# Kernel optimization log

Measured on AMD Instinct MI355X. Metric: run time of the kernel, lower is better.

## Reference

```python
import jax, jax.numpy as jnp
import numpy as np

NEG_MASK = -999.0  # matches masked_fill_(-999) in the torch source

def setup_inputs() -> dict:
    key = jax.random.key(0)
    ks = jax.random.split(key, 8)
    B, N, D = 4, 2048, 768      # batch, nodes, in_dim
    H, Do = 6, 128              # att_head, out_dim (D == H*Do)
    feat_in = jax.random.normal(ks[0], (B, N, D), dtype=jnp.float32)
    adj = jax.random.randint(ks[1], (B, N, N), 0, 2).astype(jnp.int32)
    W = jax.random.normal(ks[2], (H, D, Do), dtype=jnp.float32) * (1.0 / np.sqrt(D))
    b = jnp.zeros((Do,), dtype=jnp.float32)
    w_src = jax.random.normal(ks[3], (H, Do, 1), dtype=jnp.float32) * (1.0 / np.sqrt(Do))
    w_dst = jax.random.normal(ks[4], (H, Do, 1), dtype=jnp.float32) * (1.0 / np.sqrt(Do))
    H_w = jax.random.normal(ks[5], (D, D), dtype=jnp.float32) * (1.0 / np.sqrt(D))
    H_b = jnp.zeros((D,), dtype=jnp.float32)
    return {"feat_in": feat_in, "adj": adj, "W": W, "b": b,
            "w_src": w_src, "w_dst": w_dst, "H_w": H_w, "H_b": H_b}

def reference(feat_in, adj, W, b, w_src, w_dst, H_w, H_b):
    leaky_alpha = 0.2
    B, N, D = feat_in.shape
    Hh = W.shape[0]
    # per-head projection: [B, H, N, Do]
    h = jnp.einsum('bni,hio->bhno', feat_in, W)
    th = jnp.tanh(h)
    attn_src = jnp.einsum('bhno,hoz->bhnz', th, w_src)  # [B,H,N,1]
    attn_dst = jnp.einsum('bhno,hoz->bhnz', th, w_dst)  # [B,H,N,1]
    # additive scores: src_i + dst_j -> [B,H,N,N]
    attn = attn_src + jnp.swapaxes(attn_dst, -1, -2)
    attn = jnp.where(attn >= 0, attn, leaky_alpha * attn)
    mask = (adj == 0)[:, None, :, :]  # [B,1,N,N]
    attn = jnp.where(mask, NEG_MASK, attn)
    attn = jax.nn.softmax(attn, axis=-1)
    feat_out = jnp.einsum('bhnm,bhmo->bhno', attn, h) + b  # [B,H,N,Do]
    feat_out = jnp.swapaxes(feat_out, 1, 2).reshape(B, N, -1)  # [B,N,H*Do]
    feat_out = jax.nn.elu(feat_out)
    gate = jax.nn.sigmoid(feat_in @ H_w.T + H_b)
    out = gate * feat_out + (1.0 - gate) * feat_in
    return out
```

## Files before the change

kernel.cpp:

```cpp
#include <hip/hip_runtime.h>
#include <hip/hip_bf16.h>

#define B_ 4
#define N_ 2048
#define D_ 768
#define H_ 6
#define Do_ 128
#define M_ (B_*N_)
#define C2_ (2*D_)
#define SROW 49152

typedef __attribute__((ext_vector_type(8))) short bf16x8;
typedef __attribute__((ext_vector_type(4))) float f32x4;
typedef __attribute__((ext_vector_type(4))) int int4v;
typedef __attribute__((ext_vector_type(2))) int int2v;
typedef __attribute__((ext_vector_type(4))) float float4v;
typedef __attribute__((ext_vector_type(4))) unsigned short ushort4v;

__device__ __forceinline__ float b2f(short s){
    unsigned u = ((unsigned)(unsigned short)s) << 16;
    return __builtin_bit_cast(float, u);
}
__device__ __forceinline__ short f2b(float f){
    unsigned u = __builtin_bit_cast(unsigned, f);
    unsigned r = (u + 0x7fffu + ((u >> 16) & 1u)) >> 16;
    return (short)r;
}
__device__ __forceinline__ int pk2(float a, float b){
    unsigned ua = __builtin_bit_cast(unsigned, a) + 0x8000u;
    unsigned ub = __builtin_bit_cast(unsigned, b) + 0x8000u;
    return (int)__builtin_amdgcn_perm(ub, ua, 0x07060302u);
}
__device__ __forceinline__ float fast_tanh(float x){
    float a = fabsf(x);
    float e = __expf(-2.0f * a);
    float t = (1.0f - e) / (1.0f + e);
    return copysignf(t, x);
}

#define HT_IDX(bh, n, o) ((((size_t)((bh)*64 + ((n) >> 5))*128 + (o))*32) + ((n) & 31))

__global__ __launch_bounds__(256) void k_prep_pack(const float* __restrict__ W,
                                                   const float* __restrict__ Hw,
                                                   const int* __restrict__ adj,
                                                   short* __restrict__ bmat,
                                                   unsigned char* __restrict__ pk){
    int bid = blockIdx.x, t = threadIdx.x;
    if (bid < C2_){
        int c = bid;
        if (c < D_){
            int hd = c >> 7, o = c & 127;
            const float* wp = W + hd*D_*Do_ + o;
            for (int k = t; k < D_; k += 256) bmat[c*D_ + k] = f2b(wp[k*Do_]);
        } else {
            int d = c - D_;
            const float* hp = Hw + d*D_;
            for (int k = t; k < D_; k += 256) bmat[c*D_ + k] = f2b(hp[k]);
        }
    } else {
        int g = (bid - C2_)*256 + t;
        const int* ap = adj + (size_t)g*8;
        int4v a0 = *(const int4v*)ap;
        int4v a1 = *(const int4v*)(ap + 4);
        unsigned by = 0;
        #pragma unroll
        for (int i = 0; i < 4; i++){
            by |= (a0[i] ? 1u : 0u) << i;
            by |= (a1[i] ? 1u : 0u) << (i + 4);
        }
        pk[g] = (unsigned char)by;
    }
}

__global__ __launch_bounds__(256) void k_gemm(const float* __restrict__ A,
                                              const short* __restrict__ Bm,
                                              short* __restrict__ ht,
                                              float* outg){
    __shared__ short As[128][72];
    __shared__ short Bs[128][72];
    int lid = blockIdx.x;
    int xcd = lid & 7, s = lid >> 3;
    int bx = s >> 3, by = xcd*8 + (s & 7);
    int tid = threadIdx.x;
    int mBase = by * 128, cBase = bx * 128;
    int wave = tid >> 6, lane = tid & 63, q = lane >> 4, nL = lane & 15;
    int wr = (wave >> 1) * 64, wc = (wave & 1) * 64;
    f32x4 acc[4][4] = {};
    for (int kk = 0; kk < D_; kk += 64){
        __syncthreads();
        #pragma unroll
        for (int i = 0; i < 8; i++){
            int idx = tid + i*256;
            int row = idx >> 4, c4 = (idx & 15) * 4;
            float4v av = *(const float4v*)&A[(mBase+row)*D_ + kk + c4];
            int2v w; w[0] = pk2(av[0], av[1]); w[1] = pk2(av[2], av[3]);
            *(int2v*)&As[row][c4] = w;
        }
        #pragma unroll
        for (int i = 0; i < 4; i++){
            int idx = tid + i*256;
            int row = idx >> 3, cs = (idx & 7) * 8;
            *(int4v*)&Bs[row][cs] = *(const int4v*)&Bm[(cBase+row)*D_ + kk + cs];
        }
        __syncthreads();
        #pragma unroll
        for (int k2 = 0; k2 < 64; k2 += 32){
            bf16x8 aF[4], bF[4];
            #pragma unroll
            for (int rt = 0; rt < 4; rt++) aF[rt] = *(const bf16x8*)&As[wr + rt*16 + nL][k2 + q*8];
            #pragma unroll
            for (int ct = 0; ct < 4; ct++) bF[ct] = *(const bf16x8*)&Bs[wc + ct*16 + nL][k2 + q*8];
            #pragma unroll
            for (int rt = 0; rt < 4; rt++)
                #pragma unroll
                for (int ct = 0; ct < 4; ct++)
                    acc[rt][ct] = __builtin_amdgcn_mfma_f32_16x16x32_bf16(aF[rt], bF[ct], acc[rt][ct], 0, 0, 0);
        }
    }
    if (cBase < D_){
        int hd = cBase >> 7;
        #pragma unroll
        for (int rt = 0; rt < 4; rt++){
            #pragma unroll
            for (int ct = 0; ct < 4; ct++){
                int o  = (wc + ct*16 + nL) & 127;
                int m0 = mBase + wr + rt*16 + q*4;
                int b = m0 >> 11, n0 = m0 & 2047;
                int bh = b*H_ + hd;
                ushort4v v;
                #pragma unroll
                for (int r = 0; r < 4; r++) v[r] = (unsigned short)f2b(acc[rt][ct][r]);
                *(ushort4v*)&ht[HT_IDX(bh, n0, o)] = v;
            }
        }
    } else {
        __syncthreads();
        int dQ = cBase - D_ + wc;
        float* Ts = (float*)As + wave*1088;
        int row = lane >> 2, cbs = (lane & 3) * 16;
        #pragma unroll
        for (int rt = 0; rt < 4; rt++){
            #pragma unroll
            for (int ct = 0; ct < 4; ct++)
                #pragma unroll
                for (int r = 0; r < 4; r++)
                    Ts[(q*4 + r)*68 + ct*16 + nL] = acc[rt][ct][r];
            __builtin_amdgcn_sched_barrier(0);
            int gm = mBase + wr + rt*16 + row;
            #pragma unroll
            for (int c4 = 0; c4 < 4; c4++){
                float4v v = *(const float4v*)&Ts[row*68 + cbs + c4*4];
                *(float4v*)&outg[(size_t)gm*D_ + dQ + cbs + c4*4] = v;
            }
            __builtin_amdgcn_sched_barrier(0);
        }
    }
}

__global__ __launch_bounds__(256) void k_stats(const short* __restrict__ ht,
                                               const float* __restrict__ wsrc,
                                               const float* __restrict__ wdst,
                                               float* __restrict__ srcP,
                                               float* __restrict__ dstP){
    int g = blockIdx.x * 256 + threadIdx.x;
    int y = blockIdx.y, o0 = y * 32;
    int bh = g >> 11, n = g & 2047;
    int hd = bh % H_;
    const short* hp = ht + HT_IDX(bh, n, o0);
    const float* ws = wsrc + hd*Do_ + o0;
    const float* wd = wdst + hd*Do_ + o0;
    float as = 0.f, ad = 0.f;
    for (int o = 0; o < 32; o++){
        float t = fast_tanh(b2f(hp[o*32]));
        as += t * ws[o];
        ad += t * wd[o];
    }
    srcP[y*SROW + g] = as; dstP[y*SROW + g] = ad;
}

struct StageS {
    float E1[2048];
    float E2[2048];
    unsigned pkw[64*65];
};
struct RedS { float red[4][64][37]; };
union LdsU { StageS s; RedS r; };
__global__ __launch_bounds__(512) void k_pv(const unsigned char* __restrict__ pkG,
                                            const float* __restrict__ srcP,
                                            const float* __restrict__ dstP,
                                            const short* __restrict__ ht,
                                            const float* __restrict__ feat_in,
                                            const float* __restrict__ bias,
                                            const float* __restrict__ Hb,
                                            float* outg){
    __shared__ LdsU U;
    int lid = blockIdx.x;
    int nid = (lid & 7)*96 + (lid >> 3);
    int itile = nid & 31;
    int hd = (nid >> 5) % 6, b = nid / 192;
    int tid = threadIdx.x, wave = tid >> 6, lane = tid & 63, q = lane >> 4, nL = lane & 15;
    int rh = wave >> 1, kh = wave & 1;
    int r0 = itile * 64;
    int bh = b*H_ + hd;
    {
        const float4v* g0 = (const float4v*)(dstP + bh*N_);
        const float4v* g1 = (const float4v*)(dstP + SROW + bh*N_);
        const float4v* g2 = (const float4v*)(dstP + 2*SROW + bh*N_);
        const float4v* g3 = (const float4v*)(dstP + 3*SROW + bh*N_);
        int c4 = tid;
        float4v d = g0[c4] + g1[c4] + g2[c4] + g3[c4];
        #pragma unroll
        for (int t = 0; t < 4; t++){
            U.s.E1[c4*4 + t] = __expf(d[t]);
            U.s.E2[c4*4 + t] = __expf(0.2f * d[t]);
        }
        const unsigned* pg = (const unsigned*)(pkG + (size_t)(b*N_ + r0) * (N_/8));
        #pragma unroll
        for (int k = 0; k < 8; k++){
            int idx = tid + k*512;
            U.s.pkw[(idx >> 6)*65 + (idx & 63)] = pg[idx];
        }
    }
    __syncthreads();
    int rowL = rh*16 + nL;
    int gi = bh*N_ + r0 + rowL;
    float sv = srcP[gi] + srcP[SROW+gi] + srcP[2*SROW+gi] + srcP[3*SROW+gi];
    float e1r = __expf(sv), e2r = __expf(0.2f*sv);
    bf16x8 vone;
    #pragma unroll
    for (int t = 0; t < 8; t++) vone[t] = (short)0x3F80;
    const short* hp = ht + (size_t)bh*262144;
    f32x4 acc[8] = {};
    f32x4 accl = {};
    int base = rowL*65;
    int jEnd = kh*1024 + 1024;
    for (int j0 = kh*1024; j0 < jEnd; j0 += 32){
        unsigned by = (U.s.pkw[base + (j0 >> 5)] >> (q*8)) & 0xFF;
        int kb = j0 + q*8;
        const short* hj = hp + (size_t)(j0 >> 5)*4096 + q*8;
        float4v E1a = *(const float4v*)&U.s.E1[kb];
        float4v E1b = *(const float4v*)&U.s.E1[kb + 4];
        float4v E2a = *(const float4v*)&U.s.E2[kb];
        float4v E2b = *(const float4v*)&U.s.E2[kb + 4];
        float p[8];
        #pragma unroll
        for (int t = 0; t < 8; t++){
            float E1t = t < 4 ? E1a[t] : E1b[t-4];
            float E2t = t < 4 ? E2a[t] : E2b[t-4];
            float a = fmaxf(e1r*E1t, e2r*E2t);
            p[t] = ((by >> t) & 1u) ? a : 0.0f;
        }
        int4v pi;
        #pragma unroll
        for (int tp = 0; tp < 4; tp++) pi[tp] = pk2(p[2*tp], p[2*tp+1]);
        bf16x8 pf = __builtin_bit_cast(bf16x8, pi);
        #pragma unroll
        for (int ct = 0; ct < 8; ct++){
            bf16x8 bF = *(const bf16x8*)&hj[(ct*16 + nL)*32];
            acc[ct] = __builtin_amdgcn_mfma_f32_16x16x32_bf16(pf, bF, acc[ct], 0, 0, 0);
        }
        accl = __builtin_amdgcn_mfma_f32_16x16x32_bf16(pf, vone, accl, 0, 0, 0);
    }
    __syncthreads();
    if (kh == 1){
        #pragma unroll
        for (int ct = 0; ct < 8; ct++)
            #pragma unroll
            for (int r = 0; r < 4; r++) U.r.red[rh][lane][ct*4 + r] = acc[ct][r];
        #pragma unroll
        for (int r = 0; r < 4; r++) U.r.red[rh][lane][32 + r] = accl[r];
    }
    __syncthreads();
    if (kh == 0){
        #pragma unroll
        for (int ct = 0; ct < 8; ct++)
            #pragma unroll
            for (int r = 0; r < 4; r++) acc[ct][r] += U.r.red[rh][lane][ct*4 + r];
        #pragma unroll
        for (int r = 0; r < 4; r++) accl[r] += U.r.red[rh][lane][32 + r];
        #pragma unroll
        for (int r = 0; r < 4; r++){
            int i = r0 + rh*16 + q*4 + r;
            float invl = 1.0f / accl[r];
            size_t baseO = (size_t)(b*N_ + i)*D_ + hd*Do_;
            #pragma unroll
            for (int ct = 0; ct < 8; ct++){
                int o = ct*16 + nL;
                float v = acc[ct][r]*invl + bias[o];
                float e = v > 0.f ? v : __expf(v) - 1.0f;
                float gl = outg[baseO + o] + Hb[hd*Do_ + o];
                float g = 1.0f / (1.0f + __expf(-gl));
                float fi = feat_in[baseO + o];
                outg[baseO + o] = g*e + (1.0f - g)*fi;
            }
        }
    }
}

extern "C" void kernel_launch(void* const* d_in, const int* in_sizes, int n_in,
                              void* d_out, int out_size, void* d_ws, size_t ws_size,
                              hipStream_t stream){
    const float* feat = (const float*)d_in[0];
    const int*   adj  = (const int*)  d_in[1];
    const float* W    = (const float*)d_in[2];
    const float* bias = (const float*)d_in[3];
    const float* wsrc = (const float*)d_in[4];
    const float* wdst = (const float*)d_in[5];
    const float* Hw   = (const float*)d_in[6];
    const float* Hb   = (const float*)d_in[7];
    float* out = (float*)d_out;
    char* ws = (char*)d_ws;
    short* bmat = (short*)(ws);
    short* ht   = (short*)(ws + 2359296);
    float* srcP = (float*)(ws + 14942208);
    float* dstP = (float*)(ws + 15728640);
    unsigned char* pk = (unsigned char*)(ws + 16515072);

    hipLaunchKernelGGL(k_prep_pack, dim3(C2_ + 8192), dim3(256), 0, stream, W, Hw, adj, bmat, pk);
    hipLaunchKernelGGL(k_gemm,      dim3(768),        dim3(256), 0, stream, feat, bmat, ht, out);
    hipLaunchKernelGGL(k_stats,     dim3(192, 4),     dim3(256), 0, stream, ht, wsrc, wdst, srcP, dstP);
    hipLaunchKernelGGL(k_pv,        dim3(768),        dim3(512), 0, stream, pk, srcP, dstP,
                       ht, feat, bias, Hb, out);
}
```

Baseline: 300.8 us.

## Halve PV tile rows, drop XCD swizzle and LDS-staged gate stores in GEMM

k_pv now runs 1536 blocks of 256 threads, each covering 32 query rows instead of 64, with a launch-bounds occupancy hint and a smaller LDS footprint, aiming for more resident blocks and better load balance. k_gemm drops the XCD-aware block remapping in favour of a plain 2D grid, and writes the gate GEMM output directly from registers instead of transposing through LDS for coalesced float4 stores. Trade-offs: the dst exponent table and adjacency staging are now rebuilt by twice as many blocks, the gate stores become scattered scalar writes, and L2 locality across XCDs may get worse.

```diff
diff --git a/kernel.cpp b/kernel.cpp
--- a/kernel.cpp
+++ b/kernel.cpp
@@ -78,11 +78,8 @@
                                               float* outg){
     __shared__ short As[128][72];
     __shared__ short Bs[128][72];
-    int lid = blockIdx.x;
-    int xcd = lid & 7, s = lid >> 3;
-    int bx = s >> 3, by = xcd*8 + (s & 7);
     int tid = threadIdx.x;
-    int mBase = by * 128, cBase = bx * 128;
+    int mBase = blockIdx.y * 128, cBase = blockIdx.x * 128;
     int wave = tid >> 6, lane = tid & 63, q = lane >> 4, nL = lane & 15;
     int wr = (wave >> 1) * 64, wc = (wave & 1) * 64;
     f32x4 acc[4][4] = {};
@@ -134,25 +131,15 @@
             }
         }
     } else {
-        __syncthreads();
-        int dQ = cBase - D_ + wc;
-        float* Ts = (float*)As + wave*1088;
-        int row = lane >> 2, cbs = (lane & 3) * 16;
         #pragma unroll
         for (int rt = 0; rt < 4; rt++){
             #pragma unroll
-            for (int ct = 0; ct < 4; ct++)
+            for (int ct = 0; ct < 4; ct++){
+                int d  = cBase - D_ + wc + ct*16 + nL;
+                int m0 = mBase + wr + rt*16 + q*4;
                 #pragma unroll
-                for (int r = 0; r < 4; r++)
-                    Ts[(q*4 + r)*68 + ct*16 + nL] = acc[rt][ct][r];
-            __builtin_amdgcn_sched_barrier(0);
-            int gm = mBase + wr + rt*16 + row;
-            #pragma unroll
-            for (int c4 = 0; c4 < 4; c4++){
-                float4v v = *(const float4v*)&Ts[row*68 + cbs + c4*4];
-                *(float4v*)&outg[(size_t)gm*D_ + dQ + cbs + c4*4] = v;
+                for (int r = 0; r < 4; r++) outg[(size_t)(m0 + r)*D_ + d] = acc[rt][ct][r];
             }
-            __builtin_amdgcn_sched_barrier(0);
         }
     }
 }
@@ -181,43 +168,47 @@
 struct StageS {
     float E1[2048];
     float E2[2048];
-    unsigned pkw[64*65];
+    unsigned pkw[32*65];
 };
-struct RedS { float red[4][64][37]; };
+struct RedS { float red[2][64][37]; };
 union LdsU { StageS s; RedS r; };
-__global__ __launch_bounds__(512) void k_pv(const unsigned char* __restrict__ pkG,
-                                            const float* __restrict__ srcP,
-                                            const float* __restrict__ dstP,
-                                            const short* __restrict__ ht,
-                                            const float* __restrict__ feat_in,
-                                            const float* __restrict__ bias,
-                                            const float* __restrict__ Hb,
-                                            float* outg){
+
+__global__ __launch_bounds__(256, 6) void k_pv(const unsigned char* __restrict__ pkG,
+                                               const float* __restrict__ srcP,
+                                               const float* __restrict__ dstP,
+                                               const short* __restrict__ ht,
+                                               const float* __restrict__ feat_in,
+                                               const float* __restrict__ bias,
+                                               const float* __restrict__ Hb,
+                                               float* outg){
     __shared__ LdsU U;
     int lid = blockIdx.x;
-    int nid = (lid & 7)*96 + (lid >> 3);
-    int itile = nid & 31;
-    int hd = (nid >> 5) % 6, b = nid / 192;
+    int nid = (lid & 7)*192 + (lid >> 3);
+    int itile = nid & 63;
+    int hd = (nid >> 6) % 6, b = nid / 384;
     int tid = threadIdx.x, wave = tid >> 6, lane = tid & 63, q = lane >> 4, nL = lane & 15;
     int rh = wave >> 1, kh = wave & 1;
-    int r0 = itile * 64;
+    int r0 = itile * 32;
     int bh = b*H_ + hd;
     {
         const float4v* g0 = (const float4v*)(dstP + bh*N_);
         const float4v* g1 = (const float4v*)(dstP + SROW + bh*N_);
         const float4v* g2 = (const float4v*)(dstP + 2*SROW + bh*N_);
         const float4v* g3 = (const float4v*)(dstP + 3*SROW + bh*N_);
-        int c4 = tid;
-        float4v d = g0[c4] + g1[c4] + g2[c4] + g3[c4];
-        #pragma unroll
-        for (int t = 0; t < 4; t++){
-            U.s.E1[c4*4 + t] = __expf(d[t]);
-            U.s.E2[c4*4 + t] = __expf(0.2f * d[t]);
+        #pragma unroll
+        for (int h = 0; h < 2; h++){
+            int c4 = tid*2 + h;
+            float4v d = g0[c4] + g1[c4] + g2[c4] + g3[c4];
+            #pragma unroll
+            for (int t = 0; t < 4; t++){
+                U.s.E1[c4*4 + t] = __expf(d[t]);
+                U.s.E2[c4*4 + t] = __expf(0.2f * d[t]);
+            }
         }
         const unsigned* pg = (const unsigned*)(pkG + (size_t)(b*N_ + r0) * (N_/8));
         #pragma unroll
         for (int k = 0; k < 8; k++){
-            int idx = tid + k*512;
+            int idx = tid + k*256;
             U.s.pkw[(idx >> 6)*65 + (idx & 63)] = pg[idx];
         }
     }
@@ -317,8 +308,8 @@
     unsigned char* pk = (unsigned char*)(ws + 16515072);
 
     hipLaunchKernelGGL(k_prep_pack, dim3(C2_ + 8192), dim3(256), 0, stream, W, Hw, adj, bmat, pk);
-    hipLaunchKernelGGL(k_gemm,      dim3(768),        dim3(256), 0, stream, feat, bmat, ht, out);
+    hipLaunchKernelGGL(k_gemm,      dim3(12, 64),     dim3(256), 0, stream, feat, bmat, ht, out);
     hipLaunchKernelGGL(k_stats,     dim3(192, 4),     dim3(256), 0, stream, ht, wsrc, wdst, srcP, dstP);
-    hipLaunchKernelGGL(k_pv,        dim3(768),        dim3(512), 0, stream, pk, srcP, dstP,
+    hipLaunchKernelGGL(k_pv,        dim3(1536),       dim3(256), 0, stream, pk, srcP, dstP,
                        ht, feat, bias, Hb, out);
 }
```

New measurement: 299.8 us. Within noise of the previous version (-0.3%).
